# Optimization experiments

Hardware: AMD Instinct MI355X
Metric: run time of the kernel (lower is better)

The kernel has to match this reference:

```python
import jax, jax.numpy as jnp
import numpy as np


def setup_inputs() -> dict:
    key = jax.random.key(0)
    k1, k2, k3 = jax.random.split(key, 3)
    B, C, H, W = 8, 64, 112, 112
    kh, kw = 5, 5
    return {
        "x": jax.random.normal(k1, (B, C, H, W), dtype=jnp.float32),
        "weight": jax.random.normal(k2, (C, kh, kw), dtype=jnp.float32),
        "bias": jax.random.normal(k3, (C,), dtype=jnp.float32),
        "sign": jnp.ones((1,), dtype=jnp.float32),
        "padding": 2,
        "stride": 1,
        "func_type": 1,
        "alpha": 1,
    }


def _morpho(x, weight, bias, sign, padding, stride, func_type, alpha):
    B, C, H, W = x.shape
    kh, kw = weight.shape[-2:]
    ph = pw = padding
    sh = sw = stride
    H2 = (H + 2 * ph - kh) // sh + 1
    W2 = (W + 2 * pw - kw) // sw + 1
    # sign handling: m*sign*x + (1-m)*x == (m*sign + (1-m)) * x, m detached
    m = jax.lax.stop_gradient((jnp.abs(sign) >= 1e-7).astype(x.dtype))
    s = (m * sign + (1.0 - m)).reshape(-1, 1, 1, 1)  # broadcasts over B or is scalar
    xe = s * x
    xp = jnp.pad(xe, ((0, 0), (0, 0), (ph, ph), (pw, pw)))  # zero pad like F.unfold
    # gather sliding-window taps: [B, C, kh*kw, H2, W2]
    patches = jnp.stack(
        [xp[:, :, i : i + sh * H2 : sh, j : j + sw * W2 : sw]
         for i in range(kh) for j in range(kw)],
        axis=2,
    )
    w = weight.reshape(-1, C, kh * kw, 1, 1)  # (1 or B, C, ks, 1, 1)
    y = patches + w
    if func_type == 0:
        y = y.max(axis=2)
    elif func_type == 1:
        prob = jax.nn.softmax(alpha * y, axis=2)
        y = (y * prob).sum(axis=2)
    elif func_type == 2:
        y = jax.scipy.special.logsumexp(alpha * y, axis=2) / alpha
    else:
        raise NotImplementedError
    if bias is not None:
        y = y + bias.reshape(-1, C, 1, 1)
    y = s * y  # un-apply the sign scaling on the output
    return y  # [B, C, H2, W2]


def reference(x, weight, bias, sign, padding, stride, func_type, alpha):
    return _morpho(x, weight, bias, sign, padding, stride, func_type, alpha)
```

## Files before the change

### kernel.cpp

```cpp
#include <hip/hip_runtime.h>
#include <math.h>

typedef float v2f __attribute__((ext_vector_type(2)));

constexpr int B_  = 8;
constexpr int C_  = 64;
constexpr int H_  = 112;
constexpr int W_  = 112;
constexpr int KH  = 5;
constexpr int KW  = 5;
constexpr int PAD = 2;

constexpr int TRT = 16;
constexpr int SW  = 28;
constexpr int NSTRIP = W_ / SW;
constexpr int NT  = H_ / TRT;
constexpr int LR  = TRT + KH - 1;
constexpr int LCP = 38;
constexpr int TPB = 256;
constexpr int NITEM = LR * 9;
constexpr int NTASK = B_ * C_ * NSTRIP * NT;

__device__ __forceinline__ float uniform_f32(float v) {
    return __int_as_float(__builtin_amdgcn_readfirstlane(__float_as_int(v)));
}

__global__ __launch_bounds__(TPB)
void morpho_wave(const float* __restrict__ x,
                 const float* __restrict__ weight,
                 const float* __restrict__ bias,
                 const float* __restrict__ sign,
                 const int*   __restrict__ alpha_p,
                 float* __restrict__ out)
{
    __shared__ __align__(16) v2f sEF[4][LR][LCP];

    const int w    = threadIdx.x >> 6;
    const int lane = threadIdx.x & 63;

    const int task  = blockIdx.x * 4 + w;
    const int plane = task / (NSTRIP * NT);
    const int rem   = task - plane * (NSTRIP * NT);
    const int wgrp  = rem / NT;
    const int t     = rem - wgrp * NT;
    const int c     = plane & (C_ - 1);

    const float sg    = sign[0];
    const float seff  = (fabsf(sg) >= 1e-7f) ? sg : 1.0f;
    const float a     = (float)alpha_p[0];
    const float aK    = a * seff;
    const float inv_a = 1.0f / a;

    const float* xp  = x + (size_t)plane * (H_ * W_);
    const int    G0  = wgrp * SW;
    const int   row0 = t * TRT - PAD;

    float4 xv[3];
    int ir[3], iq[3];
#pragma unroll
    for (int k = 0; k < 3; ++k) {
        int i  = lane + 64 * k;
        int ic = (i < NITEM) ? i : (NITEM - 1);
        ir[k] = ic / 9;
        iq[k] = ic - 9 * ir[k];
        int gr = min(max(row0 + ir[k], 0), H_ - 1);
        int gb = min(max(G0 - 4 + 4 * iq[k], 0), W_ - 4);
        xv[k] = *reinterpret_cast<const float4*>(xp + gr * W_ + gb);
    }

    const float* wp = weight + c * (KH * KW);
    float su[KH * KW], sv[KH * KW];
#pragma unroll
    for (int k = 0; k < KH * KW; ++k) {
        float wv = wp[k];
        float u  = __expf(a * wv);
        su[k] = uniform_f32(u);
        sv[k] = uniform_f32(wv * u);
    }
    const float sb = seff * bias[c];

    v2f (*buf)[LCP] = sEF[w];
#pragma unroll
    for (int k = 0; k < 3; ++k) {
        int i = lane + 64 * k;
        if (i < NITEM) {
            const int r  = ir[k], q = iq[k];
            const int gr = row0 + r;
            const bool rok = (gr >= 0) && (gr < H_);
            const int cb = G0 - 4 + 4 * q;
            float4 v = xv[k];
            float ax0 = (rok && cb + 0 >= 0 && cb + 0 < W_) ? aK * v.x : 0.0f;
            float ax1 = (rok && cb + 1 >= 0 && cb + 1 < W_) ? aK * v.y : 0.0f;
            float ax2 = (rok && cb + 2 >= 0 && cb + 2 < W_) ? aK * v.z : 0.0f;
            float ax3 = (rok && cb + 3 >= 0 && cb + 3 < W_) ? aK * v.w : 0.0f;
            float e0 = __expf(ax0), e1 = __expf(ax1);
            float e2 = __expf(ax2), e3 = __expf(ax3);
            float f0 = ax0 * e0, f1 = ax1 * e1, f2 = ax2 * e2, f3 = ax3 * e3;
            float4* dst = reinterpret_cast<float4*>(&buf[r][4 * q]);
            dst[0] = make_float4(e0, f0, e1, f1);
            dst[1] = make_float4(e2, f2, e3, f3);
        }
    }

    asm volatile("s_waitcnt lgkmcnt(0)" ::: "memory");
    __builtin_amdgcn_sched_barrier(0);

    const int ty = lane >> 2;
    const int lg = lane & 3;
    const int cbase = 7 * lg;

    v2f   acc[7];
    float nm2[7];
#pragma unroll
    for (int o = 0; o < 7; ++o) { acc[o] = (v2f){0.0f, 0.0f}; nm2[o] = 0.0f; }

#pragma unroll
    for (int rr = 0; rr < KH; ++rr) {
        v2f ew[11];
#pragma unroll
        for (int jj = 0; jj < 11; ++jj) ew[jj] = buf[ty + rr][cbase + 2 + jj];
#pragma unroll
        for (int j = 0; j < KW; ++j) {
            const float u  = su[rr * 5 + j];
            const v2f   u2 = (v2f){u, u};
            const float v  = sv[rr * 5 + j];
#pragma unroll
            for (int o = 0; o < 7; ++o) {
                acc[o] = __builtin_elementwise_fma(u2, ew[o + j], acc[o]);
                nm2[o] = fmaf(v, ew[o + j].x, nm2[o]);
            }
        }
    }

    float* op = out + (size_t)plane * (H_ * W_)
                    + (size_t)(t * TRT + ty) * W_ + G0 + cbase;
#pragma unroll
    for (int o = 0; o < 7; ++o) {
        float Z   = acc[o].x;
        float num = fmaf(acc[o].y, inv_a, nm2[o]);
        op[o] = fmaf(seff * num, __builtin_amdgcn_rcpf(Z), sb);
    }
}

extern "C" void kernel_launch(void* const* d_in, const int* in_sizes, int n_in,
                              void* d_out, int out_size, void* d_ws, size_t ws_size,
                              hipStream_t stream) {
    const float* x      = (const float*)d_in[0];
    const float* weight = (const float*)d_in[1];
    const float* bias   = (const float*)d_in[2];
    const float* sign   = (const float*)d_in[3];
    const int*   alpha  = (const int*)d_in[7];
    float* out = (float*)d_out;

    dim3 grid(NTASK / 4);
    morpho_wave<<<grid, TPB, 0, stream>>>(x, weight, bias, sign, alpha, out);
}
```

Before: 27.13 us.

## Stream rows through registers per thread instead of LDS-tiled wave tasks

Replaces the shared-memory tile approach with a register-streaming design. Each block now handles one full plane, and each thread owns a 2-column strip over a 28-row segment. The thread loads three v2f per input row with a rolling 3-row prefetch, computes exp once per row, and scatters the results into a rotating set of 5 row accumulators. This removes the LDS staging and the redundant halo exponentials, but it gives up parallelism: there are 512 blocks with 224 active threads each, plus a long serial loop per thread and 8-byte strided global loads.

```diff
diff --git a/kernel.cpp b/kernel.cpp
--- a/kernel.cpp
+++ b/kernel.cpp
@@ -9,41 +9,34 @@
 constexpr int W_  = 112;
 constexpr int KH  = 5;
 constexpr int KW  = 5;
-constexpr int PAD = 2;
 
-constexpr int TRT = 16;
-constexpr int SW  = 28;
-constexpr int NSTRIP = W_ / SW;
-constexpr int NT  = H_ / TRT;
-constexpr int LR  = TRT + KH - 1;
-constexpr int LCP = 38;
-constexpr int TPB = 256;
-constexpr int NITEM = LR * 9;
-constexpr int NTASK = B_ * C_ * NSTRIP * NT;
+constexpr int SEG   = 28;
+constexpr int NSEG  = 4;
+constexpr int NPAIR = 56;
+constexpr int STEPS = SEG + KH - 1;
+constexpr int TPB   = 256;
 
 __device__ __forceinline__ float uniform_f32(float v) {
     return __int_as_float(__builtin_amdgcn_readfirstlane(__float_as_int(v)));
 }
 
 __global__ __launch_bounds__(TPB)
-void morpho_wave(const float* __restrict__ x,
-                 const float* __restrict__ weight,
-                 const float* __restrict__ bias,
-                 const float* __restrict__ sign,
-                 const int*   __restrict__ alpha_p,
-                 float* __restrict__ out)
+void morpho_stream(const float* __restrict__ x,
+                   const float* __restrict__ weight,
+                   const float* __restrict__ bias,
+                   const float* __restrict__ sign,
+                   const int*   __restrict__ alpha_p,
+                   float* __restrict__ out)
 {
-    __shared__ __align__(16) v2f sEF[4][LR][LCP];
+    const int plane = blockIdx.x;
+    const int c     = plane & (C_ - 1);
+    const int tid   = threadIdx.x;
+    if (tid >= NSEG * NPAIR) return;
 
-    const int w    = threadIdx.x >> 6;
-    const int lane = threadIdx.x & 63;
-
-    const int task  = blockIdx.x * 4 + w;
-    const int plane = task / (NSTRIP * NT);
-    const int rem   = task - plane * (NSTRIP * NT);
-    const int wgrp  = rem / NT;
-    const int t     = rem - wgrp * NT;
-    const int c     = plane & (C_ - 1);
+    const int seg = tid / NPAIR;
+    const int g   = tid - seg * NPAIR;
+    const int r0  = seg * SEG - 2;
+    const int cL  = 2 * g - 2;
 
     const float sg    = sign[0];
     const float seff  = (fabsf(sg) >= 1e-7f) ? sg : 1.0f;
@@ -51,21 +44,24 @@
     const float aK    = a * seff;
     const float inv_a = 1.0f / a;
 
-    const float* xp  = x + (size_t)plane * (H_ * W_);
-    const int    G0  = wgrp * SW;
-    const int   row0 = t * TRT - PAD;
+    const float* xp = x + (size_t)plane * (H_ * W_);
+    float*       op = out + (size_t)plane * (H_ * W_);
 
-    float4 xv[3];
-    int ir[3], iq[3];
+    const int b0 = (cL < 0) ? 0 : cL;
+    const int b1 = cL + 2;
+    const int b2 = (cL + 4 > W_ - 2) ? (W_ - 2) : (cL + 4);
+    bool cok[6];
 #pragma unroll
-    for (int k = 0; k < 3; ++k) {
-        int i  = lane + 64 * k;
-        int ic = (i < NITEM) ? i : (NITEM - 1);
-        ir[k] = ic / 9;
-        iq[k] = ic - 9 * ir[k];
-        int gr = min(max(row0 + ir[k], 0), H_ - 1);
-        int gb = min(max(G0 - 4 + 4 * iq[k], 0), W_ - 4);
-        xv[k] = *reinterpret_cast<const float4*>(xp + gr * W_ + gb);
+    for (int j = 0; j < 6; ++j) cok[j] = (cL + j >= 0) && (cL + j < W_);
+
+    v2f xv[3][3];
+#pragma unroll
+    for (int m = 0; m < 2; ++m) {
+        int gr = min(max(r0 + m, 0), H_ - 1);
+        const float* row = xp + gr * W_;
+        xv[m][0] = *reinterpret_cast<const v2f*>(row + b0);
+        xv[m][1] = *reinterpret_cast<const v2f*>(row + b1);
+        xv[m][2] = *reinterpret_cast<const v2f*>(row + b2);
     }
 
     const float* wp = weight + c * (KH * KW);
@@ -79,66 +75,73 @@
     }
     const float sb = seff * bias[c];
 
-    v2f (*buf)[LCP] = sEF[w];
+    v2f   acc[5][2];
+    float nm2[5][2];
 #pragma unroll
-    for (int k = 0; k < 3; ++k) {
-        int i = lane + 64 * k;
-        if (i < NITEM) {
-            const int r  = ir[k], q = iq[k];
-            const int gr = row0 + r;
-            const bool rok = (gr >= 0) && (gr < H_);
-            const int cb = G0 - 4 + 4 * q;
-            float4 v = xv[k];
-            float ax0 = (rok && cb + 0 >= 0 && cb + 0 < W_) ? aK * v.x : 0.0f;
-            float ax1 = (rok && cb + 1 >= 0 && cb + 1 < W_) ? aK * v.y : 0.0f;
-            float ax2 = (rok && cb + 2 >= 0 && cb + 2 < W_) ? aK * v.z : 0.0f;
-            float ax3 = (rok && cb + 3 >= 0 && cb + 3 < W_) ? aK * v.w : 0.0f;
-            float e0 = __expf(ax0), e1 = __expf(ax1);
-            float e2 = __expf(ax2), e3 = __expf(ax3);
-            float f0 = ax0 * e0, f1 = ax1 * e1, f2 = ax2 * e2, f3 = ax3 * e3;
-            float4* dst = reinterpret_cast<float4*>(&buf[r][4 * q]);
-            dst[0] = make_float4(e0, f0, e1, f1);
-            dst[1] = make_float4(e2, f2, e3, f3);
-        }
-    }
-
-    asm volatile("s_waitcnt lgkmcnt(0)" ::: "memory");
-    __builtin_amdgcn_sched_barrier(0);
-
-    const int ty = lane >> 2;
-    const int lg = lane & 3;
-    const int cbase = 7 * lg;
-
-    v2f   acc[7];
-    float nm2[7];
+    for (int s5 = 0; s5 < 5; ++s5)
 #pragma unroll
-    for (int o = 0; o < 7; ++o) { acc[o] = (v2f){0.0f, 0.0f}; nm2[o] = 0.0f; }
+        for (int c2 = 0; c2 < 2; ++c2) { acc[s5][c2] = (v2f){0.0f, 0.0f}; nm2[s5][c2] = 0.0f; }
 
 #pragma unroll
-    for (int rr = 0; rr < KH; ++rr) {
-        v2f ew[11];
+    for (int i = 0; i < STEPS; ++i) {
+        if (i + 2 < STEPS) {
+            int gr = min(max(r0 + i + 2, 0), H_ - 1);
+            const float* row = xp + gr * W_;
+            xv[(i + 2) % 3][0] = *reinterpret_cast<const v2f*>(row + b0);
+            xv[(i + 2) % 3][1] = *reinterpret_cast<const v2f*>(row + b1);
+            xv[(i + 2) % 3][2] = *reinterpret_cast<const v2f*>(row + b2);
+        }
+
+        const int  r   = r0 + i;
+        const bool rok = (r >= 0) && (r < H_);
+        v2f ew[6];
 #pragma unroll
-        for (int jj = 0; jj < 11; ++jj) ew[jj] = buf[ty + rr][cbase + 2 + jj];
+        for (int j = 0; j < 6; ++j) {
+            float xj = xv[i % 3][j >> 1][j & 1];
+            float ax = (rok && cok[j]) ? aK * xj : 0.0f;
+            float e  = __expf(ax);
+            ew[j] = (v2f){e, ax * e};
+        }
+
 #pragma unroll
-        for (int j = 0; j < KW; ++j) {
-            const float u  = su[rr * 5 + j];
-            const v2f   u2 = (v2f){u, u};
-            const float v  = sv[rr * 5 + j];
+        for (int k = 0; k < KH; ++k) {
+            const int d = i - k;
+            if (d < 0 || d >= SEG) continue;
+            const int s5 = d % 5;
 #pragma unroll
-            for (int o = 0; o < 7; ++o) {
-                acc[o] = __builtin_elementwise_fma(u2, ew[o + j], acc[o]);
-                nm2[o] = fmaf(v, ew[o + j].x, nm2[o]);
+            for (int j = 0; j < KW; ++j) {
+                const float u  = su[k * 5 + j];
+                const v2f   u2 = (v2f){u, u};
+                const float v  = sv[k * 5 + j];
+#pragma unroll
+                for (int c2 = 0; c2 < 2; ++c2) {
+                    acc[s5][c2] = __builtin_elementwise_fma(u2, ew[c2 + j], acc[s5][c2]);
+                    nm2[s5][c2] = fmaf(v, ew[c2 + j].x, nm2[s5][c2]);
+                }
             }
         }
-    }
 
-    float* op = out + (size_t)plane * (H_ * W_)
-                    + (size_t)(t * TRT + ty) * W_ + G0 + cbase;
-#pragma unroll
-    for (int o = 0; o < 7; ++o) {
-        float Z   = acc[o].x;
-        float num = fmaf(acc[o].y, inv_a, nm2[o]);
-        op[o] = fmaf(seff * num, __builtin_amdgcn_rcpf(Z), sb);
+        if (i >= 4) {
+            const int d  = i - 4;
+            const int s5 = d % 5;
+            const int ro = seg * SEG + d;
+            float v0, v1;
+            {
+                float Z   = acc[s5][0].x;
+                float num = fmaf(acc[s5][0].y, inv_a, nm2[s5][0]);
+                v0 = fmaf(seff * num, __builtin_amdgcn_rcpf(Z), sb);
+            }
+            {
+                float Z   = acc[s5][1].x;
+                float num = fmaf(acc[s5][1].y, inv_a, nm2[s5][1]);
+                v1 = fmaf(seff * num, __builtin_amdgcn_rcpf(Z), sb);
+            }
+            *reinterpret_cast<v2f*>(op + (size_t)ro * W_ + 2 * g) = (v2f){v0, v1};
+            acc[s5][0] = (v2f){0.0f, 0.0f};
+            acc[s5][1] = (v2f){0.0f, 0.0f};
+            nm2[s5][0] = 0.0f;
+            nm2[s5][1] = 0.0f;
+        }
     }
 }
 
@@ -152,6 +155,6 @@
     const int*   alpha  = (const int*)d_in[7];
     float* out = (float*)d_out;
 
-    dim3 grid(NTASK / 4);
-    morpho_wave<<<grid, TPB, 0, stream>>>(x, weight, bias, sign, alpha, out);
+    dim3 grid(B_ * C_);
+    morpho_stream<<<grid, TPB, 0, stream>>>(x, weight, bias, sign, alpha, out);
 }
```

New measurement: 26.93 us. Within noise of the previous version (-0.7%).
